# Kernel tuning notes

Measured on AMD Instinct MI355X. Metric: run time of the kernel, lower is better.

Reference implementation:

```python
import jax, jax.numpy as jnp
import numpy as np
from jax import lax

DIST_THRESH = 180.0
ATT_THRESH = 0.05


def setup_inputs() -> dict:
    key = jax.random.key(0)
    ks = jax.random.split(key, 6)
    B, N, H, W = 16, 512, 25, 25
    F, Fh = H * W, int(H * W * 1.5)  # 625, 937
    x4 = jax.random.normal(ks[0], (B, N, H, W), dtype=jnp.float32) * 0.25
    attention = jax.random.uniform(ks[1], (B, N, 1, 1), dtype=jnp.float32)
    W1 = jax.random.normal(ks[2], (2, F, Fh), dtype=jnp.float32) * (1.0 / np.sqrt(F))
    b1 = jnp.zeros((Fh,), dtype=jnp.float32)
    W2 = jax.random.normal(ks[3], (2, Fh, F), dtype=jnp.float32) * (1.0 / np.sqrt(Fh))
    b2 = jnp.zeros((F,), dtype=jnp.float32)
    return {"x4": x4, "attention": attention, "W1": W1, "b1": b1, "W2": W2, "b2": b2}


def _build_adjacency(X, att):
    """X: [B,N,F] node features, att: [B,N]. Returns thresholded adjacency [B,N,N]."""
    B, N, F = X.shape
    # pairwise L1 distances, row-by-row scan to avoid materializing [B,N,N,F]
    Xs = jnp.swapaxes(X, 0, 1)  # [N,B,F]

    def row(_, xi):  # xi: [B,F]
        d = jnp.sum(jnp.abs(xi[:, None, :] - X), axis=-1)  # [B,N]
        return None, d

    _, D = lax.scan(row, None, Xs)          # [N,B,N]
    D = jnp.swapaxes(D, 0, 1)               # [B,N,N]
    att_d = jnp.abs(att[:, :, None] - att[:, None, :])  # [B,N,N]
    A = ((D <= DIST_THRESH) & (att_d <= ATT_THRESH)).astype(jnp.float32)
    # original only fills i<j and j<i, diagonal stays 0
    A = A * (1.0 - jnp.eye(N, dtype=jnp.float32))
    return A


def _process_graph(A):
    """A + I, then row-normalize by inverse degree (D^-1 (A+I))."""
    N = A.shape[1]
    A = A + jnp.eye(N, dtype=A.dtype)
    deg = jnp.sum(A, axis=-1)               # [B,N]
    dinv = jnp.where(deg > 0, 1.0 / deg, 0.0)
    return dinv[:, :, None] * A


def _cheb_conv(x, L, Wk, b):
    """ChebConv with K=2 over dense normalized graph L: T0=x, T1=Lx."""
    t1 = jnp.einsum('bij,bjf->bif', L, x)
    return jnp.einsum('bnf,fo->bno', x, Wk[0]) + jnp.einsum('bnf,fo->bno', t1, Wk[1]) + b


def reference(x4, attention, W1, b1, W2, b2):
    B, N, H, W = x4.shape
    X = x4.reshape(B, N, H * W)             # [B,N,625] flow_x
    att = attention[:, :, 0, 0]             # [B,N]
    A = _build_adjacency(X, att)
    L = _process_graph(A)
    h = jax.nn.relu(_cheb_conv(X, L, W1, b1))   # [B,N,937]
    out = jax.nn.relu(_cheb_conv(h, L, W2, b2))  # [B,N,625]
    return out
```

## Files before the change

### kernel.cpp

```cpp
#include <hip/hip_runtime.h>
#include <stdint.h>

typedef uint16_t u16;
typedef uint32_t u32;
typedef __attribute__((ext_vector_type(4))) float f32x4;
typedef __attribute__((ext_vector_type(4))) unsigned short us4;
typedef __attribute__((ext_vector_type(8))) unsigned short us8;

#define NB   16
#define NN   512
#define FF   625
#define FH   937
#define ROWS 8192
#define KS1  1280
#define KS2  1920
#define NPX  640
#define NPH  960
#define F4   160
#define GQ   4

using frag_ab = __attribute__((ext_vector_type(8))) short;
using frag_cd = __attribute__((ext_vector_type(4))) float;

__device__ __forceinline__ u16 f32_bf16(float f) {
  union { float f; uint32_t u; } x; x.f = f;
  uint32_t r = x.u + 0x7fffu + ((x.u >> 16) & 1u);
  return (u16)(r >> 16);
}
__device__ __forceinline__ void gload_lds16(const void* g, void* l) {
  __builtin_amdgcn_global_load_lds((__attribute__((address_space(1))) void*)g,
                                   (__attribute__((address_space(3))) void*)l,
                                   16, 0, 0);
}

__global__ __launch_bounds__(256) void prep(
    const float* __restrict__ x4, const float* __restrict__ att,
    const float* __restrict__ W1, const float* __restrict__ W2,
    f32x4* __restrict__ Xpad, u16* __restrict__ Xcat, u16* __restrict__ Xt,
    u16* __restrict__ W1t, u16* __restrict__ W2t,
    u16* __restrict__ order, float* __restrict__ att_s)
{
  __shared__ __align__(16) float smem[2112];
  const int blk = blockIdx.x;
  const int tid = threadIdx.x;

  if (blk < 16) {
    float* a_sh = smem;
    const int b = blk;
    a_sh[tid]       = att[b * NN + tid];
    a_sh[tid + 256] = att[b * NN + tid + 256];
    __syncthreads();
    #pragma unroll
    for (int h = 0; h < 2; ++h) {
      const int i = tid + h * 256;
      const float ai = a_sh[i];
      int r = 0;
      for (int j = 0; j < NN; ++j) {
        const float aj = a_sh[j];
        r += (aj < ai) || (aj == ai && j < i);
      }
      order[(size_t)b * NN + r] = (u16)i;
      att_s[(size_t)b * NN + r] = ai;
    }
  } else if (blk < 1040) {
    float* T = smem;
    const int idx = blk - 16;
    const int xcd = idx & 7, sub = idx >> 3;
    const int b = xcd * 2 + (sub >> 6);
    const int rr = sub & 63;
    const int q = rr >> 4;
    const int nt = rr & 15;
    const int node0 = nt * 32;
    const int tx = tid & 31, ty = tid >> 5;
    const int lrow = tid >> 3, lcol = tid & 7;

    int buf = 0;
    {
      const int f0 = q * 160;
      #pragma unroll
      for (int r = 0; r < 4; ++r) {
        const int node = node0 + ty + r * 8;
        const int f = f0 + tx;
        T[(ty + r * 8) * 33 + tx] = (f < FF) ? x4[((size_t)b * NN + node) * FF + f] : 0.f;
      }
    }
    __syncthreads();

    for (int c = 0; c < 5; ++c) {
      const int f0 = q * 160 + c * 32;
      float vnext[4];
      const bool has = (c + 1 < 5);
      if (has) {
        const int fn = f0 + 32 + tx;
        #pragma unroll
        for (int r = 0; r < 4; ++r) {
          const int node = node0 + ty + r * 8;
          vnext[r] = (fn < FF) ? x4[((size_t)b * NN + node) * FF + fn] : 0.f;
        }
      }
      {
        const int node_l = lrow, k4s = lcol;
        const size_t grow = (size_t)b * NN + node0 + node_l;
        const int k4 = q * 40 + c * 8 + k4s;
        f32x4 v; us4 o;
        #pragma unroll
        for (int t = 0; t < 4; ++t) {
          const float x = T[buf * 1056 + node_l * 33 + k4s * 4 + t];
          v[t] = x; o[t] = f32_bf16(x);
        }
        Xpad[grow * F4 + k4] = v;
        *(us4*)(Xcat + grow * KS1 + k4 * 4) = o;
      }
      {
        const int fl = lrow, nl = lcol;
        const int f = f0 + fl;
        us4 ov;
        #pragma unroll
        for (int t = 0; t < 4; ++t)
          ov[t] = f32_bf16(T[buf * 1056 + (nl * 4 + t) * 33 + fl]);
        *(us4*)(Xt + ((size_t)b * NPX + f) * 512 + node0 + nl * 4) = ov;
      }
      if (has) {
        #pragma unroll
        for (int r = 0; r < 4; ++r)
          T[(buf ^ 1) * 1056 + (ty + r * 8) * 33 + tx] = vnext[r];
        __syncthreads();
        buf ^= 1;
      }
    }
  } else if (blk < 2320) {
    float (*tile)[33] = (float(*)[33])smem;
    const int bb = blk - 1040;
    const int kt = bb % 40, nt = bb / 40;
    const int tx = tid & 31, ty = tid >> 5;
    #pragma unroll
    for (int r = 0; r < 4; ++r) {
      int k = kt * 32 + ty + r * 8;
      int n = nt * 32 + tx;
      float v = 0.f;
      int c = -1, kk = 0;
      if (k < 625) { c = 0; kk = k; }
      else if (k >= 640 && k < 1265) { c = 1; kk = k - 640; }
      if (c >= 0 && n < FH) v = W1[((size_t)c * 625 + kk) * FH + n];
      tile[ty + r * 8][tx] = v;
    }
    __syncthreads();
    #pragma unroll
    for (int r = 0; r < 4; ++r) {
      int n = nt * 32 + ty + r * 8;
      int k = kt * 32 + tx;
      W1t[(size_t)n * KS1 + k] = f32_bf16(tile[tx][ty + r * 8]);
    }
  } else {
    float (*tile)[33] = (float(*)[33])smem;
    const int bb = blk - 2320;
    const int kt = bb % 60, nt = bb / 60;
    const int tx = tid & 31, ty = tid >> 5;
    #pragma unroll
    for (int r = 0; r < 4; ++r) {
      int k = kt * 32 + ty + r * 8;
      int n = nt * 32 + tx;
      float v = 0.f;
      int c = -1, kk = 0;
      if (k < 937) { c = 0; kk = k; }
      else if (k >= 960 && k < 1897) { c = 1; kk = k - 960; }
      if (c >= 0 && n < FF) v = W2[((size_t)c * 937 + kk) * FF + n];
      tile[ty + r * 8][tx] = v;
    }
    __syncthreads();
    #pragma unroll
    for (int r = 0; r < 4; ++r) {
      int n = nt * 32 + ty + r * 8;
      int k = kt * 32 + tx;
      W2t[(size_t)n * KS2 + k] = f32_bf16(tile[tx][ty + r * 8]);
    }
  }
}

__global__ __launch_bounds__(256) void build_L(
    const f32x4* __restrict__ Xpad,
    const u16* __restrict__ order,
    const float* __restrict__ att_s,
    u16* __restrict__ L)
{
  __shared__ float atts[512];
  __shared__ u16 ords[512];
  __shared__ u16 cand[512];
  __shared__ u16 flag[GQ][512];
  __shared__ int ncand, naccs[GQ];

  const int tid = threadIdx.x;
  const int blk = blockIdx.x;
  const int xcd = blk & 7, sub = blk >> 3;
  const int b = xcd * 2 + (sub >> 7);
  const int p0 = (sub & 127) * GQ;
  const f32x4* Xb4 = Xpad + (size_t)b * NN * F4;

  atts[tid]       = att_s[b * NN + tid];
  atts[tid + 256] = att_s[b * NN + tid + 256];
  ords[tid]       = order[b * NN + tid];
  ords[tid + 256] = order[b * NN + tid + 256];
  {
    u32* fz = (u32*)&flag[0][0];
    #pragma unroll
    for (int s = 0; s < GQ; ++s) fz[tid + s * 256] = 0;
  }
  if (tid == 0) ncand = 0;
  if (tid < GQ) naccs[tid] = 0;
  __syncthreads();

  float av[GQ]; int ig[GQ];
  #pragma unroll
  for (int g = 0; g < GQ; ++g) { av[g] = atts[p0 + g]; ig[g] = ords[p0 + g]; }
  if (tid < GQ) flag[tid][ords[p0 + tid]] = 1;

  {
    const float lo = av[0] - 0.0501f, hi = av[GQ - 1] + 0.0501f;
    const bool q0 = (atts[tid] >= lo) && (atts[tid] <= hi);
    const bool q1 = (atts[tid + 256] >= lo) && (atts[tid + 256] <= hi);
    const unsigned long long m0 = __ballot(q0);
    const unsigned long long m1 = __ballot(q1);
    const int c0 = __popcll(m0);
    const int c1 = __popcll(m1);
    const int lane = tid & 63;
    int base = 0;
    if (lane == 0 && (c0 + c1)) base = atomicAdd(&ncand, c0 + c1);
    base = __shfl(base, 0, 64);
    const unsigned long long below = (1ull << lane) - 1ull;
    if (q0) cand[base + __popcll(m0 & below)] = (u16)tid;
    if (q1) cand[base + c0 + __popcll(m1 & below)] = (u16)(tid + 256);
  }
  __syncthreads();
  const int nc = ncand;

  const int hl = tid & 31;
  const int hw = tid >> 5;

  f32x4 xi[GQ][5];
  #pragma unroll
  for (int g = 0; g < GQ; ++g) {
    const f32x4* Xi = Xb4 + (size_t)ig[g] * F4;
    #pragma unroll
    for (int s = 0; s < 5; ++s) xi[g][s] = Xi[s * 32 + hl];
  }

  for (int c = hw; c < nc; c += 8) {
    const int p = cand[c];
    const int j = ords[p];
    const float aj = atts[p];
    const f32x4* Xj = Xb4 + (size_t)j * F4;
    f32x4 xj[5];
    #pragma unroll
    for (int s = 0; s < 5; ++s) xj[s] = Xj[s * 32 + hl];

    float pd[GQ];
    #pragma unroll
    for (int g = 0; g < GQ; ++g) {
      float p2 = 0.f;
      #pragma unroll
      for (int t = 0; t < 4; ++t) {
        p2 += fabsf(xi[g][0][t] - xj[0][t]) + fabsf(xi[g][1][t] - xj[1][t])
            + fabsf(xi[g][2][t] - xj[2][t]) + fabsf(xi[g][3][t] - xj[3][t])
            + fabsf(xi[g][4][t] - xj[4][t]);
      }
      pd[g] = p2;
    }
    #pragma unroll
    for (int off = 16; off; off >>= 1) {
      #pragma unroll
      for (int g = 0; g < GQ; ++g) pd[g] += __shfl_xor(pd[g], off, 64);
    }
    if (hl == 0) {
      #pragma unroll
      for (int g = 0; g < GQ; ++g) {
        if (pd[g] <= 180.0f && fabsf(av[g] - aj) <= 0.05f && j != ig[g]) {
          flag[g][j] = 1;
          atomicAdd(&naccs[g], 1);
        }
      }
    }
  }
  __syncthreads();

  #pragma unroll
  for (int g = 0; g < GQ; ++g) {
    const u16 dv = f32_bf16(1.0f / (float)(naccs[g] + 1));
    const long row = (long)b * NN + ig[g];
    const u32 lo2 = flag[g][2 * tid]     ? (u32)dv : 0u;
    const u32 hi2 = flag[g][2 * tid + 1] ? (u32)dv : 0u;
    *(u32*)(L + (size_t)row * 512 + 2 * tid) = lo2 | (hi2 << 16);
  }
}

template <int KS, int NTILE, int NREAL, int NSTORE, bool RELU, bool BIAS,
          bool OUT_BF16, bool WT>
__device__ __forceinline__ void gemm_core(
    const u16* __restrict__ At,
    const u16* __restrict__ Btt,
    const float* __restrict__ bias, void* __restrict__ C,
    u16* __restrict__ Ct,
    long crow0, int col0, int ldc)
{
  constexpr int NI = NTILE / 32;
  constexpr int BR = NTILE / 32;
  __shared__ __align__(16) u16 Ash[128 * 64];
  __shared__ __align__(16) u16 Bsh[NTILE * 64];

  const int tid  = threadIdx.x;
  const int lane = tid & 63;
  const int wave = tid >> 6;
  const int wm = wave & 1, wn = wave >> 1;
  const int q = lane >> 4, l16 = lane & 15;

  const u16* pa[4]; const u16* pb[BR];
  #pragma unroll
  for (int r = 0; r < 4; ++r) {
    const int ci = r * 256 + tid;
    const int row = ci >> 3, cpos = ci & 7;
    pa[r] = At + (size_t)row * KS + (cpos ^ (row & 7)) * 8;
  }
  #pragma unroll
  for (int r = 0; r < BR; ++r) {
    const int ci = r * 256 + tid;
    const int row = ci >> 3, cpos = ci & 7;
    pb[r] = Btt + (size_t)row * KS + (cpos ^ (row & 7)) * 8;
  }
  const int wbase = (tid & 192) * 8;

  const frag_ab* fA[4][2]; const frag_ab* fB[NI][2];
  #pragma unroll
  for (int mi = 0; mi < 4; ++mi) {
    const int row = wm * 64 + mi * 16 + l16;
    fA[mi][0] = (const frag_ab*)&Ash[row * 64 + ((q    ) ^ (l16 & 7)) * 8];
    fA[mi][1] = (const frag_ab*)&Ash[row * 64 + ((q + 4) ^ (l16 & 7)) * 8];
  }
  #pragma unroll
  for (int ni = 0; ni < NI; ++ni) {
    const int row = wn * (NTILE / 2) + ni * 16 + l16;
    fB[ni][0] = (const frag_ab*)&Bsh[row * 64 + ((q    ) ^ (l16 & 7)) * 8];
    fB[ni][1] = (const frag_ab*)&Bsh[row * 64 + ((q + 4) ^ (l16 & 7)) * 8];
  }

  frag_cd acc[4][NI] = {};

  constexpr int KT = KS / 64;
  for (int kt = 0; kt < KT; ++kt) {
    __syncthreads();
    #pragma unroll
    for (int r = 0; r < 4; ++r) { gload_lds16(pa[r], &Ash[r * 2048 + wbase]); pa[r] += 64; }
    #pragma unroll
    for (int r = 0; r < BR; ++r) { gload_lds16(pb[r], &Bsh[r * 2048 + wbase]); pb[r] += 64; }
    __syncthreads();

    #pragma unroll
    for (int kk = 0; kk < 2; ++kk) {
      frag_ab av[4], bv[NI];
      #pragma unroll
      for (int mi = 0; mi < 4; ++mi) av[mi] = *fA[mi][kk];
      #pragma unroll
      for (int ni = 0; ni < NI; ++ni) bv[ni] = *fB[ni][kk];
      #pragma unroll
      for (int mi = 0; mi < 4; ++mi)
        #pragma unroll
        for (int ni = 0; ni < NI; ++ni)
          acc[mi][ni] = __builtin_amdgcn_mfma_f32_16x16x32_bf16(
              av[mi], bv[ni], acc[mi][ni], 0, 0, 0);
    }
  }

  #pragma unroll
  for (int ni = 0; ni < NI; ++ni) {
    const int col = col0 + wn * (NTILE / 2) + ni * 16 + l16;
    if (col >= NSTORE) continue;
    const bool ok = (col < NREAL);
    float bvv = 0.f;
    if (BIAS) bvv = ok ? bias[col] : 0.f;
    #pragma unroll
    for (int mi = 0; mi < 4; ++mi) {
      us4 tv;
      #pragma unroll
      for (int r = 0; r < 4; ++r) {
        const long rowg = crow0 + wm * 64 + mi * 16 + q * 4 + r;
        float v = acc[mi][ni][r];
        if (BIAS) v += bvv;
        if (RELU) v = fmaxf(v, 0.f);
        if (!ok) v = 0.f;
        if (OUT_BF16) {
          const u16 v16 = f32_bf16(v);
          ((u16*)C)[rowg * (size_t)ldc + col] = v16;
          if (WT) tv[r] = v16;
        } else {
          ((float*)C)[rowg * (size_t)ldc + col] = v;
        }
      }
      if (WT) {
        const long bb = crow0 >> 9;
        const int node = (int)(crow0 & 511) + wm * 64 + mi * 16 + q * 4;
        *(us4*)(Ct + ((size_t)bb * NPH + col) * 512 + node) = tv;
      }
    }
  }
}

template <int KS, int NTILE, int NREAL, int NSTORE, bool RELU, bool BIAS,
          bool OUT_BF16, bool WT>
__global__ __launch_bounds__(256) void gemm_dense(
    const u16* __restrict__ A, const u16* __restrict__ Bt,
    const float* __restrict__ bias, void* __restrict__ C,
    u16* __restrict__ Ct, int ldc)
{
  const int x = blockIdx.x;
  const int mt = ((x & 7) << 3) | (x >> 3);
  gemm_core<KS, NTILE, NREAL, NSTORE, RELU, BIAS, OUT_BF16, WT>(
      A + (size_t)mt * 128 * KS, Bt + (size_t)blockIdx.y * NTILE * KS,
      bias, C, Ct, (long)mt * 128, blockIdx.y * NTILE, ldc);
}

template <int NP>
__global__ __launch_bounds__(256) void spmm(
    const u16* __restrict__ L, const u16* __restrict__ Bt,
    u16* __restrict__ C, int ldc)
{
  constexpr int TPB = 4 * (NP / 64);
  const int blk = blockIdx.x;
  const int xcd = blk & 7, sub = blk >> 3;
  const int b = xcd * 2 + sub / TPB;
  const int t = sub % TPB;
  const int mt = t & 3, nt = t >> 2;
  gemm_core<512, 64, NP, NP, false, false, true, false>(
      L + ((size_t)b * 512 + mt * 128) * 512,
      Bt + ((size_t)b * NP + nt * 64) * 512,
      nullptr, C, nullptr, (long)b * 512 + mt * 128, nt * 64, ldc);
}

extern "C" void kernel_launch(void* const* d_in, const int* in_sizes, int n_in,
                              void* d_out, int out_size, void* d_ws, size_t ws_size,
                              hipStream_t stream) {
  const float* x4  = (const float*)d_in[0];
  const float* att = (const float*)d_in[1];
  const float* W1  = (const float*)d_in[2];
  const float* b1  = (const float*)d_in[3];
  const float* W2  = (const float*)d_in[4];
  const float* b2  = (const float*)d_in[5];
  float* out = (float*)d_out;

  char* ws = (char*)d_ws;
  f32x4* Xpad = (f32x4*)ws;
  u16* ht = (u16*)ws;       ws += (size_t)ROWS * F4 * 16;
  u16* Xcat = (u16*)ws;  ws += (size_t)ROWS * KS1 * 2;
  u16* hcat = (u16*)ws;  ws += (size_t)ROWS * KS2 * 2;
  u16* W1t  = (u16*)ws;  ws += (size_t)1024 * KS1 * 2;
  u16* W2t  = (u16*)ws;  ws += (size_t)640 * KS2 * 2;
  u16* Lm   = (u16*)ws;  ws += (size_t)NB * 512 * 512 * 2;
  u16* Xt   = (u16*)ws;  ws += (size_t)NB * NPX * 512 * 2;
  float* att_s = (float*)ws; ws += (size_t)NB * NN * 4;
  u16* order_  = (u16*)ws;   ws += (size_t)NB * NN * 2;

  prep<<<dim3(3520), 256, 0, stream>>>(x4, att, W1, W2, Xpad, Xcat, Xt,
                                       W1t, W2t, order_, att_s);
  build_L<<<dim3(2048), 256, 0, stream>>>(Xpad, order_, att_s, Lm);
  spmm<NPX><<<dim3(640), 256, 0, stream>>>(Lm, Xt, Xcat + NPX, KS1);
  gemm_dense<KS1, 64, FH, NPH, true, true, true, true><<<dim3(64, 16), 256, 0, stream>>>(
      Xcat, W1t, b1, (void*)hcat, ht, KS2);
  spmm<NPH><<<dim3(960), 256, 0, stream>>>(Lm, ht, hcat + NPH, KS2);
  gemm_dense<KS2, 64, FF, FF, true, true, false, false><<<dim3(64, 10), 256, 0, stream>>>(
      hcat, W2t, b2, (void*)out, nullptr, FF);
}
```

Before: 220.9 us.

## Replace first dense GEMM with 256x128-tile double-buffered 512-thread kernel

Adds a dedicated kernel for the first ChebConv GEMM. It uses 256x128 output tiles, 8 waves, double-buffered LDS filled by direct global-to-LDS loads with swizzle, and a grouped block-index remap for L2 locality. The aim is to raise data reuse per block and overlap loads with MFMA work, compared with the 128x64 single-stage generic gemm_dense. The grid drops to 256 blocks, so each block uses much more LDS and occupancy per CU falls. Only 256 workgroups may underfill the GPU's compute units.

```diff
diff --git a/kernel.cpp b/kernel.cpp
--- a/kernel.cpp
+++ b/kernel.cpp
@@ -5,7 +5,6 @@
 typedef uint32_t u32;
 typedef __attribute__((ext_vector_type(4))) float f32x4;
 typedef __attribute__((ext_vector_type(4))) unsigned short us4;
-typedef __attribute__((ext_vector_type(8))) unsigned short us8;
 
 #define NB   16
 #define NN   512
@@ -292,6 +291,132 @@
   }
 }
 
+__global__ __launch_bounds__(512) void gemm1_256(
+    const u16* __restrict__ A,
+    const u16* __restrict__ Bt,
+    const float* __restrict__ bias, u16* __restrict__ C,
+    u16* __restrict__ Ct)
+{
+  __shared__ __align__(16) u16 Ash[2][256 * 64];
+  __shared__ __align__(16) u16 Bsh[2][128 * 64];
+
+  const int tid  = threadIdx.x;
+  const int lane = tid & 63;
+  const int wave = tid >> 6;
+  const int wm = wave & 3;
+  const int wn = wave >> 2;
+  const int q = lane >> 4, l16 = lane & 15;
+
+  const int x = blockIdx.x;
+  const int mt = ((x & 7) << 2) | (x >> 3);
+  const int nt = blockIdx.y;
+  const u16* At  = A  + (size_t)mt * 256 * KS1;
+  const u16* Btt = Bt + (size_t)nt * 128 * KS1;
+
+  const u16* pa[4]; const u16* pb[2];
+  #pragma unroll
+  for (int r = 0; r < 4; ++r) {
+    const int ci = r * 512 + tid;
+    const int row = ci >> 3, cpos = ci & 7;
+    pa[r] = At + (size_t)row * KS1 + (cpos ^ (row & 7)) * 8;
+  }
+  #pragma unroll
+  for (int r = 0; r < 2; ++r) {
+    const int ci = r * 512 + tid;
+    const int row = ci >> 3, cpos = ci & 7;
+    pb[r] = Btt + (size_t)row * KS1 + (cpos ^ (row & 7)) * 8;
+  }
+  const int wbase = (tid & 448) * 8;
+
+  int aoff[4][2], boff[4][2];
+  #pragma unroll
+  for (int mi = 0; mi < 4; ++mi) {
+    const int row = wm * 64 + mi * 16 + l16;
+    aoff[mi][0] = row * 64 + ((q    ) ^ (l16 & 7)) * 8;
+    aoff[mi][1] = row * 64 + ((q + 4) ^ (l16 & 7)) * 8;
+  }
+  #pragma unroll
+  for (int ni = 0; ni < 4; ++ni) {
+    const int row = wn * 64 + ni * 16 + l16;
+    boff[ni][0] = row * 64 + ((q    ) ^ (l16 & 7)) * 8;
+    boff[ni][1] = row * 64 + ((q + 4) ^ (l16 & 7)) * 8;
+  }
+
+  frag_cd acc[4][4] = {};
+  constexpr int KT = KS1 / 64;
+
+  #pragma unroll
+  for (int r = 0; r < 4; ++r) { gload_lds16(pa[r], &Ash[0][r * 4096 + wbase]); pa[r] += 64; }
+  #pragma unroll
+  for (int r = 0; r < 2; ++r) { gload_lds16(pb[r], &Bsh[0][r * 4096 + wbase]); pb[r] += 64; }
+
+  int cur = 0;
+  for (int kt = 0; kt < KT; ++kt) {
+    if (kt + 1 < KT) {
+      const int nxt = cur ^ 1;
+      #pragma unroll
+      for (int r = 0; r < 4; ++r) { gload_lds16(pa[r], &Ash[nxt][r * 4096 + wbase]); pa[r] += 64; }
+      #pragma unroll
+      for (int r = 0; r < 2; ++r) { gload_lds16(pb[r], &Bsh[nxt][r * 4096 + wbase]); pb[r] += 64; }
+      asm volatile("s_waitcnt vmcnt(6)" ::: "memory");
+    } else {
+      asm volatile("s_waitcnt vmcnt(0)" ::: "memory");
+    }
+    __builtin_amdgcn_s_barrier();
+    __builtin_amdgcn_sched_barrier(0);
+
+    const u16* A0 = &Ash[cur][0];
+    const u16* B0 = &Bsh[cur][0];
+    __builtin_amdgcn_s_setprio(1);
+    #pragma unroll
+    for (int kk = 0; kk < 2; ++kk) {
+      frag_ab av[4], bv[4];
+      #pragma unroll
+      for (int mi = 0; mi < 4; ++mi) av[mi] = *(const frag_ab*)&A0[aoff[mi][kk]];
+      #pragma unroll
+      for (int ni = 0; ni < 4; ++ni) bv[ni] = *(const frag_ab*)&B0[boff[ni][kk]];
+      #pragma unroll
+      for (int mi = 0; mi < 4; ++mi)
+        #pragma unroll
+        for (int ni = 0; ni < 4; ++ni)
+          acc[mi][ni] = __builtin_amdgcn_mfma_f32_16x16x32_bf16(
+              av[mi], bv[ni], acc[mi][ni], 0, 0, 0);
+    }
+    __builtin_amdgcn_s_setprio(0);
+    __builtin_amdgcn_sched_barrier(0);
+    __builtin_amdgcn_s_barrier();
+    cur ^= 1;
+  }
+
+  const int col0 = nt * 128;
+  const long crow0 = (long)mt * 256;
+  const long bb = crow0 >> 9;
+  #pragma unroll
+  for (int ni = 0; ni < 4; ++ni) {
+    const int col = col0 + wn * 64 + ni * 16 + l16;
+    if (col >= NPH) continue;
+    const bool ok = (col < FH);
+    const float bvv = ok ? bias[col] : 0.f;
+    #pragma unroll
+    for (int mi = 0; mi < 4; ++mi) {
+      us4 tv;
+      #pragma unroll
+      for (int r = 0; r < 4; ++r) {
+        const long rowg = crow0 + wm * 64 + mi * 16 + q * 4 + r;
+        float v = acc[mi][ni][r];
+        v += bvv;
+        v = fmaxf(v, 0.f);
+        if (!ok) v = 0.f;
+        const u16 v16 = f32_bf16(v);
+        C[rowg * (size_t)KS2 + col] = v16;
+        tv[r] = v16;
+      }
+      const int node = (int)(crow0 & 511) + wm * 64 + mi * 16 + q * 4;
+      *(us4*)(Ct + ((size_t)bb * NPH + col) * 512 + node) = tv;
+    }
+  }
+}
+
 template <int KS, int NTILE, int NREAL, int NSTORE, bool RELU, bool BIAS,
           bool OUT_BF16, bool WT>
 __device__ __forceinline__ void gemm_core(
@@ -460,8 +585,7 @@
                                        W1t, W2t, order_, att_s);
   build_L<<<dim3(2048), 256, 0, stream>>>(Xpad, order_, att_s, Lm);
   spmm<NPX><<<dim3(640), 256, 0, stream>>>(Lm, Xt, Xcat + NPX, KS1);
-  gemm_dense<KS1, 64, FH, NPH, true, true, true, true><<<dim3(64, 16), 256, 0, stream>>>(
-      Xcat, W1t, b1, (void*)hcat, ht, KS2);
+  gemm1_256<<<dim3(32, 8), 512, 0, stream>>>(Xcat, W1t, b1, hcat, ht);
   spmm<NPH><<<dim3(960), 256, 0, stream>>>(Lm, ht, hcat + NPH, KS2);
   gemm_dense<KS2, 64, FF, FF, true, true, false, false><<<dim3(64, 10), 256, 0, stream>>>(
       hcat, W2t, b2, (void*)out, nullptr, FF);
```

Result: no change. 222.2 us (+0.6%).
